# Optimization experiments

Hardware: AMD Instinct MI355X
Metric: run time of the kernel (lower is better)

The kernel has to match this reference:

```python
import jax, jax.numpy as jnp
import numpy as np

NOISE = 0.1  # init kwarg `noise`

def setup_inputs() -> dict:
    key = jax.random.key(0)
    k1, k2, k3, k4 = jax.random.split(key, 4)
    B, I, S, P, O = 8, 64, 64, 16, 128
    N = B * S * P
    x = jax.random.normal(k1, (B, I, S, P), dtype=jnp.float32)
    W = jax.random.normal(k2, (O, I), dtype=jnp.float32) * 0.1
    b = jax.random.normal(k3, (O,), dtype=jnp.float32) * 0.1
    noise_eps = jax.random.normal(k4, (N, O, I), dtype=jnp.float32)
    return {"x": x, "W": W, "b": b, "noise_eps": noise_eps}

def reference(x, W, b, noise_eps):
    B, I, S, P = x.shape
    O = W.shape[0]
    # 1x1 conv2d == channel-mixing matmul + bias
    conv_out = jnp.einsum('oi,bisp->bosp', W, x) + b[None, :, None, None]
    # noised_forward: per flattened element n, weight perturbation W*noise*eps[n]
    x_flat = x.transpose(0, 2, 3, 1).reshape(-1, I)  # [N, I], N = B*S*P
    noisy = NOISE * jnp.einsum('oi,noi,ni->no', W, noise_eps, x_flat)  # [N, O]
    noisy = noisy.reshape(B, S, P, O).transpose(0, 3, 1, 2)  # [B, O, S, P]
    # noised branch is detached in the original (returns .detach())
    return conv_out + jax.lax.stop_gradient(noisy)
```

## Files before the change

kernel.cpp:

```cpp
#include <hip/hip_runtime.h>


#define NOISE 0.1f

__global__ __launch_bounds__(256) void noise_conv_kernel(
    const float* __restrict__ x,
    const float* __restrict__ W,
    const float* __restrict__ bias,
    const float* __restrict__ eps,
    float* __restrict__ out)
{
    constexpr int I = 64, O = 128, SP = 1024, NT = 16;
    __shared__ float lds_x[NT * I];
    __shared__ float lds_out[O * NT];

    const int tid = threadIdx.x;
    const int g = tid >> 4;
    const int l = tid & 15;

    const int n0  = blockIdx.x * NT;
    const int b   = n0 >> 10;
    const int sp0 = n0 & 1023;

    const float* xb = x + b * (I * SP) + sp0;
    #pragma unroll
    for (int e = tid; e < NT * I; e += 256) {
        int i = e >> 4, dn = e & 15;
        lds_x[dn * I + i] = xb[i * SP + dn];
    }

    float4 wf[8];
    #pragma unroll
    for (int k = 0; k < 8; ++k)
        wf[k] = *(const float4*)(W + (k * 16 + g) * I + l * 4);

    __syncthreads();

    const float* eps_base = eps + (size_t)n0 * 8192 + g * 64 + l * 4;

    for (int dn = 0; dn < NT; ++dn) {
        const float4 xv = *(const float4*)(lds_x + dn * I + l * 4);
        const float* ep = eps_base + dn * 8192;
        #pragma unroll
        for (int m = 0; m < 8; ++m) {
            float4 e4 = *(const float4*)(ep + m * 1024);
            float4 w4 = wf[m];
            float t0 = w4.x * xv.x, t1 = w4.y * xv.y,
                  t2 = w4.z * xv.z, t3 = w4.w * xv.w;
            float acc = t0 * fmaf(NOISE, e4.x, 1.0f)
                      + t1 * fmaf(NOISE, e4.y, 1.0f)
                      + t2 * fmaf(NOISE, e4.z, 1.0f)
                      + t3 * fmaf(NOISE, e4.w, 1.0f);
            acc += __shfl_xor(acc, 1);
            acc += __shfl_xor(acc, 2);
            acc += __shfl_xor(acc, 4);
            acc += __shfl_xor(acc, 8);
            if (l == 0)
                lds_out[(m * 16 + g) * NT + dn] = acc;
        }
    }
    __syncthreads();

    float* ob = out + b * (O * SP) + sp0;
    #pragma unroll
    for (int q = tid; q < (O * NT) / 4; q += 256) {
        int o = q >> 2, j = (q & 3) * 4;
        float4 v = *(const float4*)(lds_out + o * NT + j);
        float bo = bias[o];
        v.x += bo; v.y += bo; v.z += bo; v.w += bo;
        *(float4*)(ob + o * SP + j) = v;
    }
}

extern "C" void kernel_launch(void* const* d_in, const int* in_sizes, int n_in,
                              void* d_out, int out_size, void* d_ws, size_t ws_size,
                              hipStream_t stream) {
    const float* x    = (const float*)d_in[0];
    const float* W    = (const float*)d_in[1];
    const float* bias = (const float*)d_in[2];
    const float* eps  = (const float*)d_in[3];
    float* out = (float*)d_out;

    noise_conv_kernel<<<512, 256, 0, stream>>>(x, W, bias, eps, out);
}
```

Before: 386.0 us.

## Split output channels across blocks and halve spatial tile to raise grid size

Each block now handles 8 spatial positions and one half of the output channels instead of 16 positions and all 128 channels, so the launch grows from 512 to 2048 blocks. The aim is to fill more of the GPU's compute units and keep more memory requests in flight on the bandwidth-bound eps stream. The dn loop is also fully unrolled to expose more independent loads. In exchange, each x tile is loaded by two blocks, and the output store is narrower and uses only half the threads.

```diff
diff --git a/kernel.cpp b/kernel.cpp
--- a/kernel.cpp
+++ b/kernel.cpp
@@ -10,39 +10,45 @@
     const float* __restrict__ eps,
     float* __restrict__ out)
 {
-    constexpr int I = 64, O = 128, SP = 1024, NT = 16;
+    constexpr int I = 64, O = 128, SP = 1024;
+    constexpr int NT = 8;
+    constexpr int MH = 4;
     __shared__ float lds_x[NT * I];
-    __shared__ float lds_out[O * NT];
+    __shared__ float lds_out[MH * 16 * NT];
 
     const int tid = threadIdx.x;
     const int g = tid >> 4;
     const int l = tid & 15;
 
-    const int n0  = blockIdx.x * NT;
+    const int mh = blockIdx.x & 1;
+    const int ns = blockIdx.x >> 1;
+    const int n0  = ns * NT;
     const int b   = n0 >> 10;
     const int sp0 = n0 & 1023;
+    const int o_base = mh * 64;
 
     const float* xb = x + b * (I * SP) + sp0;
     #pragma unroll
     for (int e = tid; e < NT * I; e += 256) {
-        int i = e >> 4, dn = e & 15;
+        int i = e >> 3, dn = e & 7;
         lds_x[dn * I + i] = xb[i * SP + dn];
     }
 
-    float4 wf[8];
+    float4 wf[MH];
     #pragma unroll
-    for (int k = 0; k < 8; ++k)
-        wf[k] = *(const float4*)(W + (k * 16 + g) * I + l * 4);
+    for (int k = 0; k < MH; ++k)
+        wf[k] = *(const float4*)(W + (o_base + k * 16 + g) * I + l * 4);
 
     __syncthreads();
 
-    const float* eps_base = eps + (size_t)n0 * 8192 + g * 64 + l * 4;
+    const float* eps_base = eps + (size_t)n0 * 8192 + (o_base + g) * 64 + l * 4;
 
+    #pragma unroll
     for (int dn = 0; dn < NT; ++dn) {
         const float4 xv = *(const float4*)(lds_x + dn * I + l * 4);
         const float* ep = eps_base + dn * 8192;
         #pragma unroll
-        for (int m = 0; m < 8; ++m) {
+        for (int m = 0; m < MH; ++m) {
             float4 e4 = *(const float4*)(ep + m * 1024);
             float4 w4 = wf[m];
             float t0 = w4.x * xv.x, t1 = w4.y * xv.y,
@@ -61,14 +67,13 @@
     }
     __syncthreads();
 
-    float* ob = out + b * (O * SP) + sp0;
-    #pragma unroll
-    for (int q = tid; q < (O * NT) / 4; q += 256) {
-        int o = q >> 2, j = (q & 3) * 4;
-        float4 v = *(const float4*)(lds_out + o * NT + j);
-        float bo = bias[o];
+    float* ob = out + b * (O * SP) + o_base * SP + sp0;
+    if (tid < (MH * 16 * NT) / 4) {
+        int o_loc = tid >> 1, j = (tid & 1) * 4;
+        float4 v = *(const float4*)(lds_out + o_loc * NT + j);
+        float bo = bias[o_base + o_loc];
         v.x += bo; v.y += bo; v.z += bo; v.w += bo;
-        *(float4*)(ob + o * SP + j) = v;
+        *(float4*)(ob + o_loc * SP + j) = v;
     }
 }
 
@@ -81,5 +86,5 @@
     const float* eps  = (const float*)d_in[3];
     float* out = (float*)d_out;
 
-    noise_conv_kernel<<<512, 256, 0, stream>>>(x, W, bias, eps, out);
+    noise_conv_kernel<<<2048, 256, 0, stream>>>(x, W, bias, eps, out);
 }
```

Measured after the change: 371.0 us. 1.04x faster.
